# Optimization experiments

Measured on AMD Instinct MI355X. Metric: run time of the kernel, lower is better.

Reference implementation:

```python
import jax, jax.numpy as jnp
import numpy as np

HIDDEN = 1024
HEADS = 16
SCALE_EXP = 0.2  # module: scale = hidden_size ** (-scale)


def setup_inputs() -> dict:
    key = jax.random.key(0)
    k1, k2, k3, k4, k5 = jax.random.split(key, 5)
    b, s, h = 2, 2048, HIDDEN
    std = 1.0 / np.sqrt(h)
    return {
        "sequence_embedding": jax.random.normal(k1, (b, s, h), dtype=jnp.float32),
        "kqv_w": jax.random.normal(k2, (h, 3 * h), dtype=jnp.float32) * std,
        "kqv_b": jax.random.normal(k3, (3 * h,), dtype=jnp.float32) * std,
        "ff_w": jax.random.normal(k4, (h, h), dtype=jnp.float32) * std,
        "ff_b": jax.random.normal(k5, (h,), dtype=jnp.float32) * std,
    }


def reference(sequence_embedding, kqv_w, kqv_b, ff_w, ff_b):
    b, s, hid = sequence_embedding.shape
    d = hid // HEADS
    scale = hid ** (-SCALE_EXP)
    kqv = sequence_embedding @ kqv_w + kqv_b  # [b, s, 3h]
    k, q, v = jnp.split(kqv, 3, axis=-1)
    split_heads = lambda x: x.reshape(b, s, HEADS, d).transpose(0, 2, 1, 3)  # b h s d
    k, q, v = split_heads(k), split_heads(q), split_heads(v)
    # scores[s, n] = k_s . q_n  (rows = key pos, cols = query pos)
    scores = jnp.einsum('bhsd,bhnd->bhsn', k, q) * scale
    # faithful to source: softmax over last axis n (the QUERY axis)
    attn = jax.nn.softmax(scores, axis=-1)
    # sum over s (key positions); output indexed by n
    out = jnp.einsum('bhsn,bhsd->bhnd', attn, v)  # [b, h, s, d]
    out = out.transpose(0, 2, 1, 3).reshape(b, s, hid)
    return out @ ff_w + ff_b  # dropout is identity at inference
```

## Files before the change

kernel.cpp:

```cpp
#include <hip/hip_runtime.h>

typedef unsigned short u16;
typedef unsigned int   u32;
typedef __attribute__((ext_vector_type(8))) short s16x8;
typedef __attribute__((ext_vector_type(4))) float f32x4;

#define B_   2
#define S_   2048
#define HID  1024
#define NH   16
#define N3   3072
#define M_   4096
#define C2   0.36067376022224085f
#define OFF2 12.0f

__device__ __forceinline__ u16 f2b(float f) {
  union { float f; u32 u; } v; v.f = f;
  u32 r = (v.u + 0x7FFFu + ((v.u >> 16) & 1u)) >> 16;
  return (u16)r;
}

__device__ __forceinline__ float b2f(u16 x) {
  union { u32 u; float f; } v; v.u = (u32)x << 16;
  return v.f;
}

__device__ __forceinline__ u32 cvt_pk_bf16(float lo, float hi) {
  u32 r;
  asm("v_cvt_pk_bf16_f32 %0, %1, %2" : "=v"(r) : "v"(lo), "v"(hi));
  return r;
}

#define GLL(gp, lp)                                                          \
  __builtin_amdgcn_global_load_lds(                                          \
      (const __attribute__((address_space(1))) void*)(gp),                   \
      (__attribute__((address_space(3))) void*)(lp), 16, 0, 0)

__global__ __launch_bounds__(256) void conv_bf16(const float* __restrict__ in,
                                                 u16* __restrict__ out, int n4) {
  int i = blockIdx.x * 256 + threadIdx.x;
  if (i >= n4) return;
  float4 v = ((const float4*)in)[i];
  ushort4 o = { f2b(v.x), f2b(v.y), f2b(v.z), f2b(v.w) };
  ((ushort4*)out)[i] = o;
}

__global__ __launch_bounds__(256) void transpose_bf16(const float* __restrict__ in,
                                                      u16* __restrict__ out,
                                                      int K, int N) {
  __shared__ float T[32][33];
  const int t = threadIdx.x;
  const int k0 = blockIdx.y * 32, n0 = blockIdx.x * 32;
  {
    int r = t >> 3, c4 = (t & 7) * 4;
    float4 v = *(const float4*)(in + (size_t)(k0 + r) * N + n0 + c4);
    T[r][c4 + 0] = v.x; T[r][c4 + 1] = v.y; T[r][c4 + 2] = v.z; T[r][c4 + 3] = v.w;
  }
  __syncthreads();
  int n = t >> 3, kc = (t & 7) * 4;
  ushort4 o = { f2b(T[kc + 0][n]), f2b(T[kc + 1][n]), f2b(T[kc + 2][n]), f2b(T[kc + 3][n]) };
  *(ushort4*)(out + (size_t)(n0 + n) * K + k0 + kc) = o;
}

__global__ __launch_bounds__(256) void zero_f32(float* __restrict__ p) {
  ((float4*)p)[blockIdx.x * 256 + threadIdx.x] = (float4){0.f, 0.f, 0.f, 0.f};
}

__global__ __launch_bounds__(256) void v_transpose_scaled(const u16* __restrict__ kqv,
                                                          const float* __restrict__ zacc,
                                                          u16* __restrict__ Vtg) {
  __shared__ u16 Vl[64 * 66];
  const int t = threadIdx.x;
  const int bh = blockIdx.y, b = bh >> 4, h = bh & 15;
  const int s0 = blockIdx.x * 64;
  const u16* src = kqv + (size_t)b * S_ * N3 + 2 * HID + h * 64;
  #pragma unroll
  for (int cc = 0; cc < 2; ++cc) {
    int c = t + cc * 256;
    int row = c >> 3, dc = c & 7;
    uint4 v = *(const uint4*)(src + (size_t)(s0 + row) * N3 + dc * 8);
    u32* pe = (u32*)&v;
    #pragma unroll
    for (int e = 0; e < 4; ++e)
      *(u32*)(Vl + row * 66 + dc * 8 + 2 * e) = pe[e];
  }
  __syncthreads();
  #pragma unroll
  for (int cc = 0; cc < 2; ++cc) {
    int c = t + cc * 256;
    int d = c >> 3, sc = c & 7;
    float4 za = *(const float4*)(zacc + (size_t)bh * S_ + s0 + sc * 8);
    float4 zb = *(const float4*)(zacc + (size_t)bh * S_ + s0 + sc * 8 + 4);
    float zi[8] = { za.x, za.y, za.z, za.w, zb.x, zb.y, zb.z, zb.w };
    u16 tmp[8];
    #pragma unroll
    for (int j = 0; j < 8; ++j)
      tmp[j] = f2b(b2f(Vl[(sc * 8 + j) * 66 + d]) / zi[j]);
    *(uint4*)(Vtg + ((size_t)bh * 64 + d) * S_ + s0 + sc * 8) = *(uint4*)tmp;
  }
}

template <int OUTBF16>
__global__ __launch_bounds__(256) void gemm_bf16(const u16* __restrict__ A,
                                                 const u16* __restrict__ Bt,
                                                 const float* __restrict__ bias,
                                                 void* __restrict__ Cout,
                                                 int M, int N, int K) {
  __shared__ u16 Al[128 * 32];
  __shared__ u16 Bl[128 * 32];
  const int t = threadIdx.x, lane = t & 63, w = t >> 6;
  const int m0 = blockIdx.y * 128, n0 = blockIdx.x * 128;
  const int wm = (w >> 1) * 64, wn = (w & 1) * 64;
  const int r = lane & 15, g = lane >> 4;

  f32x4 acc[4][4];
  #pragma unroll
  for (int i = 0; i < 4; ++i)
    #pragma unroll
    for (int j = 0; j < 4; ++j) acc[i][j] = (f32x4){0.f, 0.f, 0.f, 0.f};

  const int c0 = (w << 7) + lane, c1 = c0 + 64;
  const int ar0 = c0 >> 2, ak0 = (c0 & 3) << 3;
  const int ar1 = c1 >> 2, ak1 = (c1 & 3) << 3;

  for (int k0 = 0; k0 < K; k0 += 32) {
    __syncthreads();
    GLL(A  + (size_t)(m0 + ar0) * K + k0 + ak0, Al + (w << 10));
    GLL(A  + (size_t)(m0 + ar1) * K + k0 + ak1, Al + (w << 10) + 512);
    GLL(Bt + (size_t)(n0 + ar0) * K + k0 + ak0, Bl + (w << 10));
    GLL(Bt + (size_t)(n0 + ar1) * K + k0 + ak1, Bl + (w << 10) + 512);
    __syncthreads();

    s16x8 af[4], bf[4];
    #pragma unroll
    for (int mf = 0; mf < 4; ++mf)
      af[mf] = *(const s16x8*)(Al + (wm + mf * 16 + r) * 32 + g * 8);
    #pragma unroll
    for (int nf = 0; nf < 4; ++nf)
      bf[nf] = *(const s16x8*)(Bl + (wn + nf * 16 + r) * 32 + g * 8);
    #pragma unroll
    for (int mf = 0; mf < 4; ++mf)
      #pragma unroll
      for (int nf = 0; nf < 4; ++nf)
        acc[mf][nf] = __builtin_amdgcn_mfma_f32_16x16x32_bf16(af[mf], bf[nf], acc[mf][nf], 0, 0, 0);
  }

  float bv[4];
  #pragma unroll
  for (int nf = 0; nf < 4; ++nf) bv[nf] = bias[n0 + wn + nf * 16 + r];

  #pragma unroll
  for (int mf = 0; mf < 4; ++mf)
    #pragma unroll
    for (int nf = 0; nf < 4; ++nf)
      #pragma unroll
      for (int q = 0; q < 4; ++q) {
        float o = acc[mf][nf][q] + bv[nf];
        size_t idx = (size_t)(m0 + wm + mf * 16 + 4 * g + q) * N + (n0 + wn + nf * 16 + r);
        if (OUTBF16) ((u16*)Cout)[idx] = f2b(o);
        else         ((float*)Cout)[idx] = o;
      }
}

__global__ __launch_bounds__(256) void attn_stats(const u16* __restrict__ kqv,
                                                  float* __restrict__ zacc) {
  __shared__ u16 Kl[64 * 72];
  __shared__ u16 Ql[64 * 72];
  const int t = threadIdx.x, lane = t & 63, w = t >> 6;
  const int bh = blockIdx.y, b = bh >> 4, h = bh & 15;
  const int s0 = blockIdx.x * 64;
  const int nbase = blockIdx.z * (S_ / 2);
  const u16* base = kqv + (size_t)b * S_ * N3;
  const int r = lane & 15, g = lane >> 4;

  {
    int c = t;       int row = c >> 3, dc = c & 7;
    *(uint4*)(Kl + row * 72 + dc * 8) =
        *(const uint4*)(base + (size_t)(s0 + row) * N3 + h * 64 + dc * 8);
    c = t + 256;     row = c >> 3; dc = c & 7;
    *(uint4*)(Kl + row * 72 + dc * 8) =
        *(const uint4*)(base + (size_t)(s0 + row) * N3 + h * 64 + dc * 8);
  }
  __syncthreads();
  const s16x8 ka0 = *(const s16x8*)(Kl + (w * 16 + r) * 72 + g * 8);
  const s16x8 ka1 = *(const s16x8*)(Kl + (w * 16 + r) * 72 + 32 + g * 8);

  float z[4] = {0.f, 0.f, 0.f, 0.f};

  for (int nt = 0; nt < 16; ++nt) {
    const int n0 = nbase + nt * 64;
    __syncthreads();
    {
      int c = t;       int row = c >> 3, dc = c & 7;
      *(uint4*)(Ql + row * 72 + dc * 8) =
          *(const uint4*)(base + (size_t)(n0 + row) * N3 + HID + h * 64 + dc * 8);
      c = t + 256;     row = c >> 3; dc = c & 7;
      *(uint4*)(Ql + row * 72 + dc * 8) =
          *(const uint4*)(base + (size_t)(n0 + row) * N3 + HID + h * 64 + dc * 8);
    }
    __syncthreads();

    #pragma unroll
    for (int nf = 0; nf < 4; ++nf) {
      s16x8 qb0 = *(const s16x8*)(Ql + (nf * 16 + r) * 72 + g * 8);
      s16x8 qb1 = *(const s16x8*)(Ql + (nf * 16 + r) * 72 + 32 + g * 8);
      f32x4 sc = (f32x4){0.f, 0.f, 0.f, 0.f};
      __builtin_amdgcn_s_setprio(1);
      sc = __builtin_amdgcn_mfma_f32_16x16x32_bf16(ka0, qb0, sc, 0, 0, 0);
      sc = __builtin_amdgcn_mfma_f32_16x16x32_bf16(ka1, qb1, sc, 0, 0, 0);
      __builtin_amdgcn_s_setprio(0);
      #pragma unroll
      for (int q = 0; q < 4; ++q)
        z[q] += exp2f(fmaf(sc[q], C2, -OFF2));
    }
  }
  #pragma unroll
  for (int m = 1; m <= 8; m <<= 1)
    #pragma unroll
    for (int q = 0; q < 4; ++q) z[q] += __shfl_xor(z[q], m);
  if (r == 0)
    #pragma unroll
    for (int q = 0; q < 4; ++q)
      atomicAdd(zacc + (size_t)bh * S_ + s0 + w * 16 + 4 * g + q, z[q]);
}

__global__ __launch_bounds__(256) void attn_pv(const u16* __restrict__ kqv,
                                               const u16* __restrict__ Vtg,
                                               u16* __restrict__ p0,
                                               u16* __restrict__ p1) {
  __shared__ u16 QPl[64 * 72];
  __shared__ u16 Kl[64 * 72];
  __shared__ u16 Vl[64 * 72];
  const int t = threadIdx.x, lane = t & 63, w = t >> 6;
  const int bh = blockIdx.y, b = bh >> 4, h = bh & 15;
  const int n0 = blockIdx.x * 64;
  const int sbase = blockIdx.z * 16;
  const u16* base = kqv + (size_t)b * S_ * N3;
  const u16* vtb  = Vtg + (size_t)bh * 64 * S_;
  const int r = lane & 15, g = lane >> 4;

  {
    int c = t;       int row = c >> 3, dc = c & 7;
    *(uint4*)(QPl + row * 72 + dc * 8) =
        *(const uint4*)(base + (size_t)(n0 + row) * N3 + HID + h * 64 + dc * 8);
    c = t + 256;     row = c >> 3; dc = c & 7;
    *(uint4*)(QPl + row * 72 + dc * 8) =
        *(const uint4*)(base + (size_t)(n0 + row) * N3 + HID + h * 64 + dc * 8);
  }
  __syncthreads();
  const s16x8 qa0 = *(const s16x8*)(QPl + (w * 16 + r) * 72 + g * 8);
  const s16x8 qa1 = *(const s16x8*)(QPl + (w * 16 + r) * 72 + 32 + g * 8);

  f32x4 oacc[4];
  #pragma unroll
  for (int i = 0; i < 4; ++i) oacc[i] = (f32x4){0.f, 0.f, 0.f, 0.f};

  for (int st = 0; st < 16; ++st) {
    const int s0 = (sbase + st) * 64;
    __syncthreads();
    {
      int c = t;       int row = c >> 3, dc = c & 7;
      *(uint4*)(Kl + row * 72 + dc * 8) =
          *(const uint4*)(base + (size_t)(s0 + row) * N3 + h * 64 + dc * 8);
      *(uint4*)(Vl + row * 72 + dc * 8) =
          *(const uint4*)(vtb + (size_t)row * S_ + s0 + dc * 8);
      c = t + 256;     row = c >> 3; dc = c & 7;
      *(uint4*)(Kl + row * 72 + dc * 8) =
          *(const uint4*)(base + (size_t)(s0 + row) * N3 + h * 64 + dc * 8);
      *(uint4*)(Vl + row * 72 + dc * 8) =
          *(const uint4*)(vtb + (size_t)row * S_ + s0 + dc * 8);
    }
    __syncthreads();

    #pragma unroll
    for (int sf = 0; sf < 4; ++sf) {
      f32x4 sc = (f32x4){0.f, 0.f, 0.f, 0.f};
      s16x8 kb0 = *(const s16x8*)(Kl + (sf * 16 + r) * 72 + g * 8);
      s16x8 kb1 = *(const s16x8*)(Kl + (sf * 16 + r) * 72 + 32 + g * 8);
      __builtin_amdgcn_s_setprio(1);
      sc = __builtin_amdgcn_mfma_f32_16x16x32_bf16(qa0, kb0, sc, 0, 0, 0);
      sc = __builtin_amdgcn_mfma_f32_16x16x32_bf16(qa1, kb1, sc, 0, 0, 0);
      __builtin_amdgcn_s_setprio(0);
      float pp0 = exp2f(fmaf(sc[0], C2, -OFF2));
      float pp1 = exp2f(fmaf(sc[1], C2, -OFF2));
      float pp2 = exp2f(fmaf(sc[2], C2, -OFF2));
      float pp3 = exp2f(fmaf(sc[3], C2, -OFF2));
      u32 pk01 = cvt_pk_bf16(pp0, pp1);
      u32 pk23 = cvt_pk_bf16(pp2, pp3);
      int pc = (sf * 2 + (r >> 3)) ^ (2 * g);
      int pbase = (w * 16 + 4 * g) * 72 + pc * 8 + (r & 7);
      QPl[pbase]       = (u16)pk01;
      QPl[pbase + 72]  = (u16)(pk01 >> 16);
      QPl[pbase + 144] = (u16)pk23;
      QPl[pbase + 216] = (u16)(pk23 >> 16);
    }
    __builtin_amdgcn_s_setprio(1);
    #pragma unroll
    for (int ks = 0; ks < 2; ++ks) {
      s16x8 pa = *(const s16x8*)(QPl + (w * 16 + r) * 72 +
                                 ((ks * 4 + g) ^ (2 * (r >> 2))) * 8);
      #pragma unroll
      for (int df = 0; df < 4; ++df) {
        s16x8 vb = *(const s16x8*)(Vl + (df * 16 + r) * 72 + ks * 32 + g * 8);
        oacc[df] = __builtin_amdgcn_mfma_f32_16x16x32_bf16(pa, vb, oacc[df], 0, 0, 0);
      }
    }
    __builtin_amdgcn_s_setprio(0);
  }

  u16* dst = blockIdx.z ? p1 : p0;
  #pragma unroll
  for (int df = 0; df < 4; ++df)
    #pragma unroll
    for (int q = 0; q < 4; ++q)
      dst[(size_t)(b * S_ + n0 + w * 16 + 4 * g + q) * HID + h * 64 + df * 16 + r] =
          f2b(oacc[df][q]);
}

__global__ __launch_bounds__(256) void combine_halves(u16* __restrict__ p0,
                                                      const u16* __restrict__ p1) {
  int i = blockIdx.x * 256 + threadIdx.x;
  uint4 a = ((const uint4*)p0)[i];
  uint4 bq = ((const uint4*)p1)[i];
  const u16* ae = (const u16*)&a;
  const u16* be = (const u16*)&bq;
  u16 o[8];
  #pragma unroll
  for (int j = 0; j < 8; ++j) o[j] = f2b(b2f(ae[j]) + b2f(be[j]));
  ((uint4*)p0)[i] = *(uint4*)o;
}

extern "C" void kernel_launch(void* const* d_in, const int* in_sizes, int n_in,
                              void* d_out, int out_size, void* d_ws, size_t ws_size,
                              hipStream_t stream) {
  const float* x     = (const float*)d_in[0];
  const float* kqv_w = (const float*)d_in[1];
  const float* kqv_b = (const float*)d_in[2];
  const float* ff_w  = (const float*)d_in[3];
  const float* ff_b  = (const float*)d_in[4];
  float* out = (float*)d_out;

  u16* xb    = (u16*)d_ws;
  u16* w1t   = xb   + (size_t)M_ * HID;
  u16* w2t   = w1t  + (size_t)N3 * HID;
  u16* kqvb  = w2t  + (size_t)HID * HID;
  u16* vtg   = kqvb + (size_t)M_ * N3;
  float* zac = (float*)(vtg + (size_t)B_ * NH * 64 * S_);
  u16* attnb = (u16*)(zac + (size_t)B_ * NH * S_);

  dim3 blk(256);
  conv_bf16<<<dim3(M_ * HID / 4 / 256), blk, 0, stream>>>(x, xb, M_ * HID / 4);
  transpose_bf16<<<dim3(N3 / 32, HID / 32), blk, 0, stream>>>(kqv_w, w1t, HID, N3);
  transpose_bf16<<<dim3(HID / 32, HID / 32), blk, 0, stream>>>(ff_w, w2t, HID, HID);

  gemm_bf16<1><<<dim3(N3 / 128, M_ / 128), blk, 0, stream>>>(
      xb, w1t, kqv_b, kqvb, M_, N3, HID);

  zero_f32<<<dim3(B_ * NH * S_ / 4 / 256), blk, 0, stream>>>(zac);
  attn_stats<<<dim3(S_ / 64, B_ * NH, 2), blk, 0, stream>>>(kqvb, zac);
  v_transpose_scaled<<<dim3(S_ / 64, B_ * NH), blk, 0, stream>>>(kqvb, zac, vtg);
  attn_pv<<<dim3(S_ / 64, B_ * NH, 2), blk, 0, stream>>>(kqvb, vtg, attnb, xb);
  combine_halves<<<dim3(M_ * HID / 8 / 256), blk, 0, stream>>>(attnb, xb);

  gemm_bf16<0><<<dim3(HID / 128, M_ / 128), blk, 0, stream>>>(
      attnb, w2t, ff_b, out, M_, HID, HID);
}
```

Measured before the change: 201.8 us.

## Load K/Q/V MFMA fragments directly from global memory, dropping LDS staging

Both attention kernels stop staging K, Q and V tiles through shared memory behind block barriers. Each wave now loads its MFMA operand fragments straight from global memory, relying on L1/L2 caches for the reuse across waves. LDS stays only for the P tile in attn_pv, and launch-bounds occupancy hints are added. This removes the __syncthreads stalls and LDS traffic, but each wave now issues redundant global loads with less coalesced access, and the P-tile LDS path in attn_pv loses its barriers.

```diff
diff --git a/kernel.cpp b/kernel.cpp
--- a/kernel.cpp
+++ b/kernel.cpp
@@ -162,10 +162,8 @@
       }
 }
 
-__global__ __launch_bounds__(256) void attn_stats(const u16* __restrict__ kqv,
-                                                  float* __restrict__ zacc) {
-  __shared__ u16 Kl[64 * 72];
-  __shared__ u16 Ql[64 * 72];
+__global__ __launch_bounds__(256, 6) void attn_stats(const u16* __restrict__ kqv,
+                                                     float* __restrict__ zacc) {
   const int t = threadIdx.x, lane = t & 63, w = t >> 6;
   const int bh = blockIdx.y, b = bh >> 4, h = bh & 15;
   const int s0 = blockIdx.x * 64;
@@ -173,64 +171,44 @@
   const u16* base = kqv + (size_t)b * S_ * N3;
   const int r = lane & 15, g = lane >> 4;
 
-  {
-    int c = t;       int row = c >> 3, dc = c & 7;
-    *(uint4*)(Kl + row * 72 + dc * 8) =
-        *(const uint4*)(base + (size_t)(s0 + row) * N3 + h * 64 + dc * 8);
-    c = t + 256;     row = c >> 3; dc = c & 7;
-    *(uint4*)(Kl + row * 72 + dc * 8) =
-        *(const uint4*)(base + (size_t)(s0 + row) * N3 + h * 64 + dc * 8);
-  }
-  __syncthreads();
-  const s16x8 ka0 = *(const s16x8*)(Kl + (w * 16 + r) * 72 + g * 8);
-  const s16x8 ka1 = *(const s16x8*)(Kl + (w * 16 + r) * 72 + 32 + g * 8);
-
+  const u16* kp = base + (size_t)(s0 + w * 16 + r) * N3 + h * 64 + g * 8;
+  const s16x8 ka0 = *(const s16x8*)(kp);
+  const s16x8 ka1 = *(const s16x8*)(kp + 32);
+
+  const u16* qp = base + (size_t)(nbase + r) * N3 + HID + h * 64 + g * 8;
   float z[4] = {0.f, 0.f, 0.f, 0.f};
 
   for (int nt = 0; nt < 16; ++nt) {
-    const int n0 = nbase + nt * 64;
-    __syncthreads();
-    {
-      int c = t;       int row = c >> 3, dc = c & 7;
-      *(uint4*)(Ql + row * 72 + dc * 8) =
-          *(const uint4*)(base + (size_t)(n0 + row) * N3 + HID + h * 64 + dc * 8);
-      c = t + 256;     row = c >> 3; dc = c & 7;
-      *(uint4*)(Ql + row * 72 + dc * 8) =
-          *(const uint4*)(base + (size_t)(n0 + row) * N3 + HID + h * 64 + dc * 8);
-    }
-    __syncthreads();
-
     #pragma unroll
     for (int nf = 0; nf < 4; ++nf) {
-      s16x8 qb0 = *(const s16x8*)(Ql + (nf * 16 + r) * 72 + g * 8);
-      s16x8 qb1 = *(const s16x8*)(Ql + (nf * 16 + r) * 72 + 32 + g * 8);
+      const u16* q = qp + (size_t)(nt * 64 + nf * 16) * N3;
+      s16x8 qb0 = *(const s16x8*)(q);
+      s16x8 qb1 = *(const s16x8*)(q + 32);
       f32x4 sc = (f32x4){0.f, 0.f, 0.f, 0.f};
       __builtin_amdgcn_s_setprio(1);
       sc = __builtin_amdgcn_mfma_f32_16x16x32_bf16(ka0, qb0, sc, 0, 0, 0);
       sc = __builtin_amdgcn_mfma_f32_16x16x32_bf16(ka1, qb1, sc, 0, 0, 0);
       __builtin_amdgcn_s_setprio(0);
       #pragma unroll
-      for (int q = 0; q < 4; ++q)
-        z[q] += exp2f(fmaf(sc[q], C2, -OFF2));
+      for (int q2 = 0; q2 < 4; ++q2)
+        z[q2] += exp2f(fmaf(sc[q2], C2, -OFF2));
     }
   }
   #pragma unroll
   for (int m = 1; m <= 8; m <<= 1)
     #pragma unroll
-    for (int q = 0; q < 4; ++q) z[q] += __shfl_xor(z[q], m);
+    for (int q2 = 0; q2 < 4; ++q2) z[q2] += __shfl_xor(z[q2], m);
   if (r == 0)
     #pragma unroll
-    for (int q = 0; q < 4; ++q)
-      atomicAdd(zacc + (size_t)bh * S_ + s0 + w * 16 + 4 * g + q, z[q]);
-}
-
-__global__ __launch_bounds__(256) void attn_pv(const u16* __restrict__ kqv,
-                                               const u16* __restrict__ Vtg,
-                                               u16* __restrict__ p0,
-                                               u16* __restrict__ p1) {
-  __shared__ u16 QPl[64 * 72];
-  __shared__ u16 Kl[64 * 72];
-  __shared__ u16 Vl[64 * 72];
+    for (int q2 = 0; q2 < 4; ++q2)
+      atomicAdd(zacc + (size_t)bh * S_ + s0 + w * 16 + 4 * g + q2, z[q2]);
+}
+
+__global__ __launch_bounds__(256, 4) void attn_pv(const u16* __restrict__ kqv,
+                                                  const u16* __restrict__ Vtg,
+                                                  u16* __restrict__ p0,
+                                                  u16* __restrict__ p1) {
+  __shared__ u16 Pl[64 * 72];
   const int t = threadIdx.x, lane = t & 63, w = t >> 6;
   const int bh = blockIdx.y, b = bh >> 4, h = bh & 15;
   const int n0 = blockIdx.x * 64;
@@ -239,17 +217,12 @@
   const u16* vtb  = Vtg + (size_t)bh * 64 * S_;
   const int r = lane & 15, g = lane >> 4;
 
-  {
-    int c = t;       int row = c >> 3, dc = c & 7;
-    *(uint4*)(QPl + row * 72 + dc * 8) =
-        *(const uint4*)(base + (size_t)(n0 + row) * N3 + HID + h * 64 + dc * 8);
-    c = t + 256;     row = c >> 3; dc = c & 7;
-    *(uint4*)(QPl + row * 72 + dc * 8) =
-        *(const uint4*)(base + (size_t)(n0 + row) * N3 + HID + h * 64 + dc * 8);
-  }
-  __syncthreads();
-  const s16x8 qa0 = *(const s16x8*)(QPl + (w * 16 + r) * 72 + g * 8);
-  const s16x8 qa1 = *(const s16x8*)(QPl + (w * 16 + r) * 72 + 32 + g * 8);
+  const u16* qp = base + (size_t)(n0 + w * 16 + r) * N3 + HID + h * 64 + g * 8;
+  const s16x8 qa0 = *(const s16x8*)(qp);
+  const s16x8 qa1 = *(const s16x8*)(qp + 32);
+
+  const u16* kp = base + (size_t)r * N3 + h * 64 + g * 8;
+  const u16* vp = vtb + (size_t)r * S_ + g * 8;
 
   f32x4 oacc[4];
   #pragma unroll
@@ -257,26 +230,13 @@
 
   for (int st = 0; st < 16; ++st) {
     const int s0 = (sbase + st) * 64;
-    __syncthreads();
-    {
-      int c = t;       int row = c >> 3, dc = c & 7;
-      *(uint4*)(Kl + row * 72 + dc * 8) =
-          *(const uint4*)(base + (size_t)(s0 + row) * N3 + h * 64 + dc * 8);
-      *(uint4*)(Vl + row * 72 + dc * 8) =
-          *(const uint4*)(vtb + (size_t)row * S_ + s0 + dc * 8);
-      c = t + 256;     row = c >> 3; dc = c & 7;
-      *(uint4*)(Kl + row * 72 + dc * 8) =
-          *(const uint4*)(base + (size_t)(s0 + row) * N3 + h * 64 + dc * 8);
-      *(uint4*)(Vl + row * 72 + dc * 8) =
-          *(const uint4*)(vtb + (size_t)row * S_ + s0 + dc * 8);
-    }
-    __syncthreads();
 
     #pragma unroll
     for (int sf = 0; sf < 4; ++sf) {
+      const u16* k = kp + (size_t)(s0 + sf * 16) * N3;
+      s16x8 kb0 = *(const s16x8*)(k);
+      s16x8 kb1 = *(const s16x8*)(k + 32);
       f32x4 sc = (f32x4){0.f, 0.f, 0.f, 0.f};
-      s16x8 kb0 = *(const s16x8*)(Kl + (sf * 16 + r) * 72 + g * 8);
-      s16x8 kb1 = *(const s16x8*)(Kl + (sf * 16 + r) * 72 + 32 + g * 8);
       __builtin_amdgcn_s_setprio(1);
       sc = __builtin_amdgcn_mfma_f32_16x16x32_bf16(qa0, kb0, sc, 0, 0, 0);
       sc = __builtin_amdgcn_mfma_f32_16x16x32_bf16(qa1, kb1, sc, 0, 0, 0);
@@ -289,19 +249,19 @@
       u32 pk23 = cvt_pk_bf16(pp2, pp3);
       int pc = (sf * 2 + (r >> 3)) ^ (2 * g);
       int pbase = (w * 16 + 4 * g) * 72 + pc * 8 + (r & 7);
-      QPl[pbase]       = (u16)pk01;
-      QPl[pbase + 72]  = (u16)(pk01 >> 16);
-      QPl[pbase + 144] = (u16)pk23;
-      QPl[pbase + 216] = (u16)(pk23 >> 16);
+      Pl[pbase]       = (u16)pk01;
+      Pl[pbase + 72]  = (u16)(pk01 >> 16);
+      Pl[pbase + 144] = (u16)pk23;
+      Pl[pbase + 216] = (u16)(pk23 >> 16);
     }
     __builtin_amdgcn_s_setprio(1);
     #pragma unroll
     for (int ks = 0; ks < 2; ++ks) {
-      s16x8 pa = *(const s16x8*)(QPl + (w * 16 + r) * 72 +
+      s16x8 pa = *(const s16x8*)(Pl + (w * 16 + r) * 72 +
                                  ((ks * 4 + g) ^ (2 * (r >> 2))) * 8);
       #pragma unroll
       for (int df = 0; df < 4; ++df) {
-        s16x8 vb = *(const s16x8*)(Vl + (df * 16 + r) * 72 + ks * 32 + g * 8);
+        s16x8 vb = *(const s16x8*)(vp + (size_t)(df * 16) * S_ + s0 + ks * 32);
         oacc[df] = __builtin_amdgcn_mfma_f32_16x16x32_bf16(pa, vb, oacc[df], 0, 0, 0);
       }
     }
```

New measurement: 487.4 us. 141% more time.
